# Kernel tuning notes

Hardware: AMD Instinct MI355X
Metric: run time of the kernel (lower is better)

Reference implementation:

```python
import jax, jax.numpy as jnp
import numpy as np


def setup_inputs() -> dict:
    key = jax.random.key(0)
    kq, kk, kv = jax.random.split(key, 3)
    B, H, T, D = 2, 8, 8192, 64
    return {
        "Q": jax.random.normal(kq, (B, H, T, D), dtype=jnp.float32),
        "K": jax.random.normal(kk, (B, H, T, D), dtype=jnp.float32),
        "V": jax.random.normal(kv, (B, H, T, D), dtype=jnp.float32),
        "window_size": 512,
    }


def _gather_bands(x, nb, Wn):
    # x: [B,H,T,D] -> [B,H,nb,3*Wn,D], key blocks (i-1, i, i+1) per query block i
    B, H, T, D = x.shape
    xb = x.reshape(B, H, nb, Wn, D)
    xp = jnp.pad(xb, ((0, 0), (0, 0), (1, 1), (0, 0), (0, 0)))
    return jnp.concatenate([xp[:, :, i:i + nb] for i in range(3)], axis=3)


def reference(Q, K, V, window_size):
    # Sliding-window attention: softmax over keys with |q_idx - kv_idx| <= window_size,
    # computed block-sparsely (only the 3 neighboring key blocks per query block).
    B, H, T, D = Q.shape
    Wn = int(window_size)
    assert T % Wn == 0
    nb = T // Wn
    scale = 1.0 / (D ** 0.5)

    Qb = Q.reshape(B, H, nb, Wn, D)
    Kw = _gather_bands(K, nb, Wn)  # [B,H,nb,3W,D]
    Vw = _gather_bands(V, nb, Wn)

    # scores within the band: [B,H,nb,W,3W]
    s = jnp.einsum('bhnqd,bhnkd->bhnqk', Qb, Kw) * scale

    # exact band mask: global q = n*W + q_loc, global kv = (n-1)*W + k_loc
    q_loc = jnp.arange(Wn)[:, None]
    k_loc = jnp.arange(3 * Wn)[None, :]
    band = jnp.abs(q_loc + Wn - k_loc) <= Wn          # [W, 3W]
    kv_g = (jnp.arange(nb)[:, None] - 1) * Wn + jnp.arange(3 * Wn)[None, :]  # [nb, 3W]
    valid = (kv_g >= 0) & (kv_g < T)
    mask = band[None, :, :] & valid[:, None, :]        # [nb, W, 3W]

    s = jnp.where(mask[None, None], s, -jnp.inf)
    p = jax.nn.softmax(s, axis=-1)
    o = jnp.einsum('bhnqk,bhnkd->bhnqd', p, Vw)
    return o.reshape(B, H, T, D)
```

## Files before the change

kernel.cpp:

```cpp
#include <hip/hip_runtime.h>
#include <hip/hip_bf16.h>
#include <stdint.h>

typedef __attribute__((ext_vector_type(8))) short bf16x8;
typedef __attribute__((ext_vector_type(4))) short bf16x4;
typedef __attribute__((ext_vector_type(4))) float f32x4;

#define T_SEQ   8192
#define D_HEAD  64
#define NHEADS  16
#define WIN     512
#define BQ      128
#define BK      64
#define NTILES  (T_SEQ / BK)
#define LDSR    72
#define VTR     65
#define MASKVAL (-1.0e6f)

#define MFMA16(a,b,c) __builtin_amdgcn_mfma_f32_16x16x16bf16_1k(a,b,c,0,0,0)

extern "C" __device__ __attribute__((const)) float __ocml_native_exp2_f32(float);
__device__ __forceinline__ float fexp2(float x) { return __ocml_native_exp2_f32(x); }

__device__ __forceinline__ short f2bf(float f) {
    union { float f; uint32_t u; } v; v.f = f;
    return (short)((v.u + 0x7FFFu + ((v.u >> 16) & 1u)) >> 16);
}

__device__ __forceinline__ uint32_t pkbf2(float lo, float hi) {
    union { __hip_bfloat162 h; uint32_t u; } c;
    c.h = __float22bfloat162_rn(make_float2(lo, hi));
    return c.u;
}

__global__ __launch_bounds__(256, 4)
void swa_fused(const float* __restrict__ Qg, const float* __restrict__ Kg,
               const float* __restrict__ Vg, float* __restrict__ Og)
{
    __shared__ short Ks[BK * LDSR];
    __shared__ short Vs[D_HEAD * LDSR];
    __shared__ float Vtmp[BK * VTR];

    const int tid  = threadIdx.x;
    const int wave = tid >> 6;
    const int lane = tid & 63;
    const int lcol = lane & 15;
    const int quad = lane >> 4;

    const int g    = blockIdx.x;
    const int head = g >> 6;
    const int qt   = ((g & 7) << 3) | ((g >> 3) & 7);
    const int q0   = qt * BQ;
    const int tq   = q0 >> 6;

    const size_t hoff = (size_t)head * T_SEQ * D_HEAD;
    const float* Qp = Qg + hoff;
    const float* Kp = Kg + hoff;
    const float* Vp = Vg + hoff;
    float*       Op = Og + hoff;

    const float qscale = 0.125f * 1.44269504088896340736f;
    const int qrow_w = q0 + wave * 32;

    bf16x8 qf[2][2];
    #pragma unroll
    for (int mt = 0; mt < 2; ++mt) {
        const float* qptr = Qp + (size_t)(qrow_w + mt*16 + lcol) * D_HEAD + quad * 8;
        #pragma unroll
        for (int ks = 0; ks < 2; ++ks) {
            float4 a = *(const float4*)(qptr + ks*32);
            float4 b = *(const float4*)(qptr + ks*32 + 4);
            bf16x8 f;
            f[0]=f2bf(a.x*qscale); f[1]=f2bf(a.y*qscale); f[2]=f2bf(a.z*qscale); f[3]=f2bf(a.w*qscale);
            f[4]=f2bf(b.x*qscale); f[5]=f2bf(b.y*qscale); f[6]=f2bf(b.z*qscale); f[7]=f2bf(b.w*qscale);
            qf[mt][ks] = f;
        }
    }

    f32x4 oacc[2][4];
    float l_run[2];
    const f32x4 zero4 = {0.f, 0.f, 0.f, 0.f};
    #pragma unroll
    for (int mt = 0; mt < 2; ++mt) {
        l_run[mt] = 0.f;
        #pragma unroll
        for (int nt = 0; nt < 4; ++nt) oacc[mt][nt] = zero4;
    }

    int t0 = (q0 - WIN) >> 6;            if (t0 < 0) t0 = 0;
    int t1 = (q0 + BQ - 1 + WIN) >> 6;   if (t1 > NTILES - 1) t1 = NTILES - 1;

    const int krow0 = tid >> 3, kc = (tid & 7) << 3;
    const int krow1 = krow0 + 32;
    const int vrow  = tid >> 4, vc = (tid & 15) << 2;
    const int td    = tid >> 2, tkq = (tid & 3) << 4;

    for (int t = t0; t <= t1; ++t) {
        const float* ksrc = Kp + (size_t)t * BK * D_HEAD;
        const float* vsrc = Vp + (size_t)t * BK * D_HEAD;
        float4 k00 = *(const float4*)(ksrc + krow0*D_HEAD + kc);
        float4 k01 = *(const float4*)(ksrc + krow0*D_HEAD + kc + 4);
        float4 k10 = *(const float4*)(ksrc + krow1*D_HEAD + kc);
        float4 k11 = *(const float4*)(ksrc + krow1*D_HEAD + kc + 4);
        float4 v0  = *(const float4*)(vsrc + (vrow     )*D_HEAD + vc);
        float4 v1  = *(const float4*)(vsrc + (vrow + 16)*D_HEAD + vc);
        float4 v2  = *(const float4*)(vsrc + (vrow + 32)*D_HEAD + vc);
        float4 v3  = *(const float4*)(vsrc + (vrow + 48)*D_HEAD + vc);

        __syncthreads();

        *(float4*)&Vtmp[(vrow     )*VTR + vc] = v0;
        *(float4*)&Vtmp[(vrow + 16)*VTR + vc] = v1;
        *(float4*)&Vtmp[(vrow + 32)*VTR + vc] = v2;
        *(float4*)&Vtmp[(vrow + 48)*VTR + vc] = v3;
        *(int4*)&Ks[krow0*LDSR + kc] = make_int4((int)pkbf2(k00.x,k00.y), (int)pkbf2(k00.z,k00.w),
                                                 (int)pkbf2(k01.x,k01.y), (int)pkbf2(k01.z,k01.w));
        *(int4*)&Ks[krow1*LDSR + kc] = make_int4((int)pkbf2(k10.x,k10.y), (int)pkbf2(k10.z,k10.w),
                                                 (int)pkbf2(k11.x,k11.y), (int)pkbf2(k11.z,k11.w));

        __syncthreads();

        {
            uint32_t w0 = pkbf2(Vtmp[(tkq+ 0)*VTR + td], Vtmp[(tkq+ 1)*VTR + td]);
            uint32_t w1 = pkbf2(Vtmp[(tkq+ 2)*VTR + td], Vtmp[(tkq+ 3)*VTR + td]);
            uint32_t w2 = pkbf2(Vtmp[(tkq+ 4)*VTR + td], Vtmp[(tkq+ 5)*VTR + td]);
            uint32_t w3 = pkbf2(Vtmp[(tkq+ 6)*VTR + td], Vtmp[(tkq+ 7)*VTR + td]);
            uint32_t w4 = pkbf2(Vtmp[(tkq+ 8)*VTR + td], Vtmp[(tkq+ 9)*VTR + td]);
            uint32_t w5 = pkbf2(Vtmp[(tkq+10)*VTR + td], Vtmp[(tkq+11)*VTR + td]);
            uint32_t w6 = pkbf2(Vtmp[(tkq+12)*VTR + td], Vtmp[(tkq+13)*VTR + td]);
            uint32_t w7 = pkbf2(Vtmp[(tkq+14)*VTR + td], Vtmp[(tkq+15)*VTR + td]);
            *(int4*)&Vs[td*LDSR + tkq]     = make_int4((int)w0,(int)w1,(int)w2,(int)w3);
            *(int4*)&Vs[td*LDSR + tkq + 8] = make_int4((int)w4,(int)w5,(int)w6,(int)w7);
        }

        __syncthreads();

        const bool edge = (t < tq - 6) || (t > tq + 7);

        #pragma unroll
        for (int h = 0; h < 2; ++h) {
            f32x4 sc[2][2];
            #pragma unroll
            for (int j = 0; j < 2; ++j) { sc[j][0] = zero4; sc[j][1] = zero4; }
            #pragma unroll
            for (int ks = 0; ks < 2; ++ks) {
                #pragma unroll
                for (int j = 0; j < 2; ++j) {
                    bf16x8 kf = *(const bf16x8*)&Ks[((2*h+j)*16 + lcol)*LDSR + ks*32 + quad*8];
                    sc[j][0] = __builtin_amdgcn_mfma_f32_16x16x32_bf16(kf, qf[0][ks], sc[j][0], 0,0,0);
                    sc[j][1] = __builtin_amdgcn_mfma_f32_16x16x32_bf16(kf, qf[1][ks], sc[j][1], 0,0,0);
                }
            }

            if (edge) {
                #pragma unroll
                for (int j = 0; j < 2; ++j) {
                    const int kg0 = t*BK + (2*h+j)*16 + quad*4;
                    #pragma unroll
                    for (int mt = 0; mt < 2; ++mt) {
                        const int qg = qrow_w + mt*16 + lcol;
                        #pragma unroll
                        for (int r = 0; r < 4; ++r) {
                            int dq = qg - (kg0 + r);
                            if (dq > WIN || dq < -WIN) sc[j][mt][r] = MASKVAL;
                        }
                    }
                }
            }

            #pragma unroll
            for (int j = 0; j < 2; ++j) {
                const int kt = 2*h + j;
                bf16x4 vf[4];
                #pragma unroll
                for (int nt = 0; nt < 4; ++nt)
                    vf[nt] = *(const bf16x4*)&Vs[(nt*16 + lcol)*LDSR + kt*16 + quad*4];
                #pragma unroll
                for (int mt = 0; mt < 2; ++mt) {
                    float p0 = fexp2(sc[j][mt][0]);
                    float p1 = fexp2(sc[j][mt][1]);
                    float p2 = fexp2(sc[j][mt][2]);
                    float p3 = fexp2(sc[j][mt][3]);
                    l_run[mt] += (p0 + p1) + (p2 + p3);
                    union { int2 i; bf16x4 v; } pf;
                    pf.i = make_int2((int)pkbf2(p0, p1), (int)pkbf2(p2, p3));
                    #pragma unroll
                    for (int nt = 0; nt < 4; ++nt)
                        oacc[mt][nt] = MFMA16(vf[nt], pf.v, oacc[mt][nt]);
                }
            }
        }
    }

    #pragma unroll
    for (int mt = 0; mt < 2; ++mt) {
        float l = l_run[mt];
        l += __shfl_xor(l, 16, 64);
        l += __shfl_xor(l, 32, 64);
        float inv = 1.0f / l;
        const int qg = qrow_w + mt*16 + lcol;
        float* op = Op + (size_t)qg * D_HEAD + quad*4;
        #pragma unroll
        for (int nt = 0; nt < 4; ++nt) {
            float4 o = { oacc[mt][nt][0]*inv, oacc[mt][nt][1]*inv,
                         oacc[mt][nt][2]*inv, oacc[mt][nt][3]*inv };
            *(float4*)(op + nt*16) = o;
        }
    }
}

extern "C" void kernel_launch(void* const* d_in, const int* in_sizes, int n_in,
                              void* d_out, int out_size, void* d_ws, size_t ws_size,
                              hipStream_t stream)
{
    (void)in_sizes; (void)n_in; (void)out_size; (void)d_ws; (void)ws_size;
    const float* Q = (const float*)d_in[0];
    const float* K = (const float*)d_in[1];
    const float* V = (const float*)d_in[2];
    float* O = (float*)d_out;
    swa_fused<<<dim3(NHEADS * (T_SEQ / BQ)), dim3(256), 0, stream>>>(Q, K, V, O);
}
```

Measured before the change: 202.9 us.

## Precompute bf16 K and transposed bf16 V tiles in a prep kernel

```diff
diff --git a/kernel.cpp b/kernel.cpp
--- a/kernel.cpp
+++ b/kernel.cpp
@@ -14,8 +14,9 @@
 #define BK      64
 #define NTILES  (T_SEQ / BK)
 #define LDSR    72
-#define VTR     65
 #define MASKVAL (-1.0e6f)
+
+#define WS_NEEDED ((size_t)2 * NHEADS * T_SEQ * D_HEAD * 2)
 
 #define MFMA16(a,b,c) __builtin_amdgcn_mfma_f32_16x16x16bf16_1k(a,b,c,0,0,0)
 
@@ -33,13 +34,201 @@
     return c.u;
 }
 
+__global__ __launch_bounds__(256, 2)
+void prep_kv(const float* __restrict__ Kg, const float* __restrict__ Vg,
+             short* __restrict__ Kb, short* __restrict__ Vt)
+{
+    __shared__ float vt[64 * 65];
+    const int tid  = threadIdx.x;
+    const int tile = blockIdx.x & (NTILES - 1);
+    const int head = blockIdx.x >> 7;
+    const size_t off = ((size_t)head * T_SEQ + (size_t)tile * BK) * D_HEAD;
+
+    const float* ks = Kg + off;
+    short* kd = Kb + off;
+    #pragma unroll
+    for (int i = 0; i < 4; ++i) {
+        int idx = tid + 256 * i;
+        float4 v = *(const float4*)(ks + idx * 4);
+        short4 h = { f2bf(v.x), f2bf(v.y), f2bf(v.z), f2bf(v.w) };
+        *(short4*)(kd + idx * 4) = h;
+    }
+
+    const float* vs = Vg + off;
+    #pragma unroll
+    for (int i = 0; i < 4; ++i) {
+        int idx = tid + 256 * i;
+        int row = idx >> 4, c4 = (idx & 15) << 2;
+        float4 v = *(const float4*)(vs + row * D_HEAD + c4);
+        *(float4*)&vt[row * 65 + c4] = v;
+    }
+    __syncthreads();
+    short* vd = Vt + ((size_t)head * NTILES + tile) * (BK * D_HEAD);
+    {
+        int d = tid >> 2, kq = (tid & 3) << 4;
+        short out[16];
+        #pragma unroll
+        for (int j = 0; j < 16; ++j) out[j] = f2bf(vt[(kq + j) * 65 + d]);
+        *(bf16x8*)(vd + d * BK + kq)     = *(bf16x8*)&out[0];
+        *(bf16x8*)(vd + d * BK + kq + 8) = *(bf16x8*)&out[8];
+    }
+}
+
 __global__ __launch_bounds__(256, 4)
-void swa_fused(const float* __restrict__ Qg, const float* __restrict__ Kg,
-               const float* __restrict__ Vg, float* __restrict__ Og)
+void swa_fwd(const float* __restrict__ Qg, const short* __restrict__ Kb,
+             const short* __restrict__ Vt, float* __restrict__ Og)
 {
     __shared__ short Ks[BK * LDSR];
     __shared__ short Vs[D_HEAD * LDSR];
-    __shared__ float Vtmp[BK * VTR];
+
+    const int tid  = threadIdx.x;
+    const int wave = tid >> 6;
+    const int lane = tid & 63;
+    const int lcol = lane & 15;
+    const int quad = lane >> 4;
+
+    const int g    = blockIdx.x;
+    const int head = (g >> 3) >> 3;
+    const int qt   = ((g & 7) << 3) | ((g >> 3) & 7);
+    const int q0   = qt * BQ;
+    const int tq   = q0 >> 6;
+
+    const float* Qp = Qg + (size_t)head * T_SEQ * D_HEAD;
+    const short* Kp = Kb + (size_t)head * T_SEQ * D_HEAD;
+    float*       Op = Og + (size_t)head * T_SEQ * D_HEAD;
+
+    const float qscale = 0.125f * 1.44269504088896340736f;
+    const int qrow_w = q0 + wave * 32;
+
+    bf16x8 qf[2][2];
+    #pragma unroll
+    for (int mt = 0; mt < 2; ++mt) {
+        const float* qptr = Qp + (size_t)(qrow_w + mt*16 + lcol) * D_HEAD + quad * 8;
+        #pragma unroll
+        for (int ks = 0; ks < 2; ++ks) {
+            float4 a = *(const float4*)(qptr + ks*32);
+            float4 b = *(const float4*)(qptr + ks*32 + 4);
+            bf16x8 f;
+            f[0]=f2bf(a.x*qscale); f[1]=f2bf(a.y*qscale); f[2]=f2bf(a.z*qscale); f[3]=f2bf(a.w*qscale);
+            f[4]=f2bf(b.x*qscale); f[5]=f2bf(b.y*qscale); f[6]=f2bf(b.z*qscale); f[7]=f2bf(b.w*qscale);
+            qf[mt][ks] = f;
+        }
+    }
+
+    f32x4 oacc[2][4];
+    float l_run[2];
+    const f32x4 zero4 = {0.f, 0.f, 0.f, 0.f};
+    #pragma unroll
+    for (int mt = 0; mt < 2; ++mt) {
+        l_run[mt] = 0.f;
+        #pragma unroll
+        for (int nt = 0; nt < 4; ++nt) oacc[mt][nt] = zero4;
+    }
+
+    int t0 = (q0 - WIN) >> 6;            if (t0 < 0) t0 = 0;
+    int t1 = (q0 + BQ - 1 + WIN) >> 6;   if (t1 > NTILES - 1) t1 = NTILES - 1;
+
+    const int srow0 = tid >> 3, sc0 = (tid & 7) << 3;
+    const int srow1 = srow0 + 32;
+
+    for (int t = t0; t <= t1; ++t) {
+        const short* ksrc = Kp + (size_t)t * BK * D_HEAD;
+        const short* vsrc = Vt + ((size_t)head * NTILES + t) * (BK * D_HEAD);
+        bf16x8 k0 = *(const bf16x8*)(ksrc + tid * 8);
+        bf16x8 k1 = *(const bf16x8*)(ksrc + (tid + 256) * 8);
+        bf16x8 v0 = *(const bf16x8*)(vsrc + tid * 8);
+        bf16x8 v1 = *(const bf16x8*)(vsrc + (tid + 256) * 8);
+
+        __syncthreads();
+
+        *(bf16x8*)&Ks[srow0 * LDSR + sc0] = k0;
+        *(bf16x8*)&Ks[srow1 * LDSR + sc0] = k1;
+        *(bf16x8*)&Vs[srow0 * LDSR + sc0] = v0;
+        *(bf16x8*)&Vs[srow1 * LDSR + sc0] = v1;
+
+        __syncthreads();
+
+        const bool edge = (t < tq - 6) || (t > tq + 7);
+
+        #pragma unroll
+        for (int h = 0; h < 2; ++h) {
+            f32x4 sc[2][2];
+            #pragma unroll
+            for (int j = 0; j < 2; ++j) { sc[j][0] = zero4; sc[j][1] = zero4; }
+            #pragma unroll
+            for (int ks = 0; ks < 2; ++ks) {
+                #pragma unroll
+                for (int j = 0; j < 2; ++j) {
+                    bf16x8 kf = *(const bf16x8*)&Ks[((2*h+j)*16 + lcol)*LDSR + ks*32 + quad*8];
+                    sc[j][0] = __builtin_amdgcn_mfma_f32_16x16x32_bf16(kf, qf[0][ks], sc[j][0], 0,0,0);
+                    sc[j][1] = __builtin_amdgcn_mfma_f32_16x16x32_bf16(kf, qf[1][ks], sc[j][1], 0,0,0);
+                }
+            }
+
+            if (edge) {
+                #pragma unroll
+                for (int j = 0; j < 2; ++j) {
+                    const int kg0 = t*BK + (2*h+j)*16 + quad*4;
+                    #pragma unroll
+                    for (int mt = 0; mt < 2; ++mt) {
+                        const int qg = qrow_w + mt*16 + lcol;
+                        #pragma unroll
+                        for (int r = 0; r < 4; ++r) {
+                            int dq = qg - (kg0 + r);
+                            if (dq > WIN || dq < -WIN) sc[j][mt][r] = MASKVAL;
+                        }
+                    }
+                }
+            }
+
+            #pragma unroll
+            for (int j = 0; j < 2; ++j) {
+                const int kt = 2*h + j;
+                bf16x4 vf[4];
+                #pragma unroll
+                for (int nt = 0; nt < 4; ++nt)
+                    vf[nt] = *(const bf16x4*)&Vs[(nt*16 + lcol)*LDSR + kt*16 + quad*4];
+                #pragma unroll
+                for (int mt = 0; mt < 2; ++mt) {
+                    float p0 = fexp2(sc[j][mt][0]);
+                    float p1 = fexp2(sc[j][mt][1]);
+                    float p2 = fexp2(sc[j][mt][2]);
+                    float p3 = fexp2(sc[j][mt][3]);
+                    l_run[mt] += (p0 + p1) + (p2 + p3);
+                    union { int2 i; bf16x4 v; } pf;
+                    pf.i = make_int2((int)pkbf2(p0, p1), (int)pkbf2(p2, p3));
+                    #pragma unroll
+                    for (int nt = 0; nt < 4; ++nt)
+                        oacc[mt][nt] = MFMA16(vf[nt], pf.v, oacc[mt][nt]);
+                }
+            }
+        }
+    }
+
+    #pragma unroll
+    for (int mt = 0; mt < 2; ++mt) {
+        float l = l_run[mt];
+        l += __shfl_xor(l, 16, 64);
+        l += __shfl_xor(l, 32, 64);
+        float inv = 1.0f / l;
+        const int qg = qrow_w + mt*16 + lcol;
+        float* op = Op + (size_t)qg * D_HEAD + quad*4;
+        #pragma unroll
+        for (int nt = 0; nt < 4; ++nt) {
+            float4 o = { oacc[mt][nt][0]*inv, oacc[mt][nt][1]*inv,
+                         oacc[mt][nt][2]*inv, oacc[mt][nt][3]*inv };
+            *(float4*)(op + nt*16) = o;
+        }
+    }
+}
+
+__global__ __launch_bounds__(256, 4)
+void swa_fused_fb(const float* __restrict__ Qg, const float* __restrict__ Kg,
+                  const float* __restrict__ Vg, float* __restrict__ Og)
+{
+    __shared__ short Ks[BK * LDSR];
+    __shared__ short Vs[D_HEAD * LDSR];
+    __shared__ float Vtmp[BK * 65];
 
     const int tid  = threadIdx.x;
     const int wave = tid >> 6;
@@ -109,10 +298,10 @@
 
         __syncthreads();
 
-        *(float4*)&Vtmp[(vrow     )*VTR + vc] = v0;
-        *(float4*)&Vtmp[(vrow + 16)*VTR + vc] = v1;
-        *(float4*)&Vtmp[(vrow + 32)*VTR + vc] = v2;
-        *(float4*)&Vtmp[(vrow + 48)*VTR + vc] = v3;
+        *(float4*)&Vtmp[(vrow     )*65 + vc] = v0;
+        *(float4*)&Vtmp[(vrow + 16)*65 + vc] = v1;
+        *(float4*)&Vtmp[(vrow + 32)*65 + vc] = v2;
+        *(float4*)&Vtmp[(vrow + 48)*65 + vc] = v3;
         *(int4*)&Ks[krow0*LDSR + kc] = make_int4((int)pkbf2(k00.x,k00.y), (int)pkbf2(k00.z,k00.w),
                                                  (int)pkbf2(k01.x,k01.y), (int)pkbf2(k01.z,k01.w));
         *(int4*)&Ks[krow1*LDSR + kc] = make_int4((int)pkbf2(k10.x,k10.y), (int)pkbf2(k10.z,k10.w),
@@ -121,14 +310,14 @@
         __syncthreads();
 
         {
-            uint32_t w0 = pkbf2(Vtmp[(tkq+ 0)*VTR + td], Vtmp[(tkq+ 1)*VTR + td]);
-            uint32_t w1 = pkbf2(Vtmp[(tkq+ 2)*VTR + td], Vtmp[(tkq+ 3)*VTR + td]);
-            uint32_t w2 = pkbf2(Vtmp[(tkq+ 4)*VTR + td], Vtmp[(tkq+ 5)*VTR + td]);
-            uint32_t w3 = pkbf2(Vtmp[(tkq+ 6)*VTR + td], Vtmp[(tkq+ 7)*VTR + td]);
-            uint32_t w4 = pkbf2(Vtmp[(tkq+ 8)*VTR + td], Vtmp[(tkq+ 9)*VTR + td]);
-            uint32_t w5 = pkbf2(Vtmp[(tkq+10)*VTR + td], Vtmp[(tkq+11)*VTR + td]);
-            uint32_t w6 = pkbf2(Vtmp[(tkq+12)*VTR + td], Vtmp[(tkq+13)*VTR + td]);
-            uint32_t w7 = pkbf2(Vtmp[(tkq+14)*VTR + td], Vtmp[(tkq+15)*VTR + td]);
+            uint32_t w0 = pkbf2(Vtmp[(tkq+ 0)*65 + td], Vtmp[(tkq+ 1)*65 + td]);
+            uint32_t w1 = pkbf2(Vtmp[(tkq+ 2)*65 + td], Vtmp[(tkq+ 3)*65 + td]);
+            uint32_t w2 = pkbf2(Vtmp[(tkq+ 4)*65 + td], Vtmp[(tkq+ 5)*65 + td]);
+            uint32_t w3 = pkbf2(Vtmp[(tkq+ 6)*65 + td], Vtmp[(tkq+ 7)*65 + td]);
+            uint32_t w4 = pkbf2(Vtmp[(tkq+ 8)*65 + td], Vtmp[(tkq+ 9)*65 + td]);
+            uint32_t w5 = pkbf2(Vtmp[(tkq+10)*65 + td], Vtmp[(tkq+11)*65 + td]);
+            uint32_t w6 = pkbf2(Vtmp[(tkq+12)*65 + td], Vtmp[(tkq+13)*65 + td]);
+            uint32_t w7 = pkbf2(Vtmp[(tkq+14)*65 + td], Vtmp[(tkq+15)*65 + td]);
             *(int4*)&Vs[td*LDSR + tkq]     = make_int4((int)w0,(int)w1,(int)w2,(int)w3);
             *(int4*)&Vs[td*LDSR + tkq + 8] = make_int4((int)w4,(int)w5,(int)w6,(int)w7);
         }
@@ -213,10 +402,17 @@
                               void* d_out, int out_size, void* d_ws, size_t ws_size,
                               hipStream_t stream)
 {
-    (void)in_sizes; (void)n_in; (void)out_size; (void)d_ws; (void)ws_size;
     const float* Q = (const float*)d_in[0];
     const float* K = (const float*)d_in[1];
     const float* V = (const float*)d_in[2];
     float* O = (float*)d_out;
-    swa_fused<<<dim3(NHEADS * (T_SEQ / BQ)), dim3(256), 0, stream>>>(Q, K, V, O);
-}
+
+    if (ws_size >= WS_NEEDED) {
+        short* Kb = (short*)d_ws;
+        short* Vt = Kb + (size_t)NHEADS * T_SEQ * D_HEAD;
+        prep_kv<<<dim3(NHEADS * NTILES), dim3(256), 0, stream>>>(K, V, Kb, Vt);
+        swa_fwd<<<dim3(NHEADS * (T_SEQ / BQ)), dim3(256), 0, stream>>>(Q, Kb, Vt, O);
+    } else {
+        swa_fused_fb<<<dim3(NHEADS * (T_SEQ / BQ)), dim3(256), 0, stream>>>(Q, K, V, O);
+    }
+}
```

Measured after the change: 181.0 us. 1.12x faster.
